# Performance work log

Hardware: AMD Instinct MI355X
Metric: run time of the kernel (lower is better)

Reference implementation:

```python
import jax, jax.numpy as jnp
import numpy as np

B, S, D_IN, D_OUT, H = 2, 2048, 1024, 1024, 16
HEAD = D_OUT // H

def setup_inputs() -> dict:
    key = jax.random.key(0)
    ks = jax.random.split(key, 5)
    scale = 0.02
    return {
        "x": jax.random.normal(ks[0], (B, S, D_IN), dtype=jnp.float32),
        "Wq": jax.random.normal(ks[1], (D_OUT, D_IN), dtype=jnp.float32) * scale,
        "Wk": jax.random.normal(ks[2], (D_OUT, D_IN), dtype=jnp.float32) * scale,
        "Wv": jax.random.normal(ks[3], (D_OUT, D_IN), dtype=jnp.float32) * scale,
        "Wo": jax.random.normal(ks[4], (D_OUT, D_OUT), dtype=jnp.float32) * scale,
        "bo": jnp.zeros((D_OUT,), dtype=jnp.float32),
    }

def reference(x, Wq, Wk, Wv, Wo, bo):
    b, n, _ = x.shape
    # linear projections (torch Linear: y = x @ W.T)
    q = (x @ Wq.T).reshape(b, n, H, HEAD).transpose(0, 2, 1, 3)  # [b,h,n,d]
    k = (x @ Wk.T).reshape(b, n, H, HEAD).transpose(0, 2, 1, 3)
    v = (x @ Wv.T).reshape(b, n, H, HEAD).transpose(0, 2, 1, 3)
    scores = jnp.einsum('bhqd,bhkd->bhqk', q, k)  # [b,h,n,n]
    causal = jnp.triu(jnp.ones((n, n), dtype=bool), k=1)
    scores = jnp.where(causal, -jnp.inf, scores)
    # NOTE: original scales by sqrt(d_out**0.5) == d_out**0.25 (faithful quirk)
    inv_scale = jnp.float32(1.0 / (D_OUT ** 0.25))
    attn = jax.nn.softmax(scores * inv_scale, axis=-1)
    ctx = jnp.einsum('bhqk,bhkd->bhqd', attn, v)  # [b,h,n,d]
    ctx = ctx.transpose(0, 2, 1, 3).reshape(b, n, D_OUT)
    return ctx @ Wo.T + bo
```

## Files before the change

### kernel.cpp

```cpp
#include <hip/hip_runtime.h>

#define NB 2
#define NH 16
#define SEQ 2048
#define DM 1024
#define HD 64
#define MT (NB * SEQ)

typedef __attribute__((ext_vector_type(8))) short bf16x8;
typedef __attribute__((ext_vector_type(4))) float f32x4;
typedef __attribute__((ext_vector_type(8))) unsigned short ushort8;

__device__ __forceinline__ unsigned short f2bf(float f) {
  union { float f; unsigned u; } v; v.f = f;
  return (unsigned short)((v.u + 0x7fffu + ((v.u >> 16) & 1u)) >> 16);
}

__device__ __forceinline__ void gld_lds16(const unsigned short* g, unsigned short* l) {
  __builtin_amdgcn_global_load_lds((const __attribute__((address_space(1))) unsigned int*)g,
                                   (__attribute__((address_space(3))) unsigned int*)l, 16, 0, 0);
}

__global__ __launch_bounds__(256) void cvt_all(const float* __restrict__ x,
                                               const float* __restrict__ wq,
                                               const float* __restrict__ wk,
                                               const float* __restrict__ wv,
                                               const float* __restrict__ wo,
                                               unsigned short* __restrict__ dst) {
  const int XO = (MT * DM) / 8;
  const int WO = (DM * DM) / 8;
  int i = blockIdx.x * 256 + threadIdx.x;
  const float* src; int base;
  if (i < XO)               { src = x;  base = 0; }
  else if (i < XO + WO)     { src = wq; base = XO; }
  else if (i < XO + 2 * WO) { src = wk; base = XO + WO; }
  else if (i < XO + 3 * WO) { src = wv; base = XO + 2 * WO; }
  else                      { src = wo; base = XO + 3 * WO; }
  const float4* s4 = (const float4*)(src) + (size_t)(i - base) * 2;
  float4 f0 = s4[0], f1 = s4[1];
  ushort8 u;
  u[0] = f2bf(f0.x); u[1] = f2bf(f0.y); u[2] = f2bf(f0.z); u[3] = f2bf(f0.w);
  u[4] = f2bf(f1.x); u[5] = f2bf(f1.y); u[6] = f2bf(f1.z); u[7] = f2bf(f1.w);
  *((ushort8*)dst + i) = u;
}

#define QSCALE 0.2550565444f

__global__ __launch_bounds__(128, 2) void gemm_qkv(const unsigned short* __restrict__ xb,
                                                   const unsigned short* __restrict__ wcat,
                                                   unsigned short* __restrict__ qb,
                                                   unsigned short* __restrict__ kb,
                                                   unsigned short* __restrict__ vtb) {
  __shared__ unsigned short As[128 * 64], Bs[128 * 64];
  int m0 = blockIdx.y * 128, n0 = blockIdx.x * 128;
  int tid = threadIdx.x, lane = tid & 63, l15 = lane & 15, quad = lane >> 4, w = tid >> 6;
  const unsigned short* A = xb + (size_t)m0 * DM;
  const unsigned short* B = wcat + (size_t)n0 * DM;

  int gofs[8];
#pragma unroll
  for (int it = 0; it < 8; ++it) {
    int c = tid + it * 128;
    int r = c >> 3, pos = c & 7;
    gofs[it] = r * DM + ((pos ^ (r & 7)) * 8);
  }

  f32x4 acc[8][4];
#pragma unroll
  for (int j = 0; j < 8; ++j)
#pragma unroll
    for (int i = 0; i < 4; ++i) acc[j][i] = (f32x4){0.f, 0.f, 0.f, 0.f};

  for (int k0 = 0; k0 < DM; k0 += 64) {
#pragma unroll
    for (int it = 0; it < 8; ++it)
      gld_lds16(A + k0 + gofs[it], As + (tid + it * 128) * 8);
#pragma unroll
    for (int it = 0; it < 8; ++it)
      gld_lds16(B + k0 + gofs[it], Bs + (tid + it * 128) * 8);
    __syncthreads();
#pragma unroll
    for (int s = 0; s < 2; ++s) {
      bf16x8 fa[4];
#pragma unroll
      for (int i = 0; i < 4; ++i) {
        int row = w * 64 + i * 16 + l15, sw = row & 7;
        fa[i] = *(const bf16x8*)(As + row * 64 + (((quad + 4 * s) ^ sw) * 8));
      }
#pragma unroll
      for (int j = 0; j < 8; ++j) {
        int row = j * 16 + l15, sw = row & 7;
        bf16x8 fb = *(const bf16x8*)(Bs + row * 64 + (((quad + 4 * s) ^ sw) * 8));
#pragma unroll
        for (int i = 0; i < 4; ++i)
          acc[j][i] = __builtin_amdgcn_mfma_f32_16x16x32_bf16(fb, fa[i], acc[j][i], 0, 0, 0);
      }
    }
    __syncthreads();
  }

  int mat = n0 >> 10;
#pragma unroll
  for (int j = 0; j < 8; ++j) {
#pragma unroll
    for (int i = 0; i < 4; ++i) {
      int n = n0 + j * 16 + quad * 4;
      int m = m0 + w * 64 + i * 16 + l15;
      int bi = m >> 11, s = m & 2047;
      int c = n & 1023, h = c >> 6, d0 = c & 63;
      if (mat == 2) {
#pragma unroll
        for (int reg = 0; reg < 4; ++reg)
          vtb[((size_t)((bi * NH + h) * HD + d0 + reg)) * SEQ + s] = f2bf(acc[j][i][reg]);
      } else {
        unsigned short* dst = (mat == 0) ? qb : kb;
        float sc = (mat == 0) ? QSCALE : 1.0f;
        ushort4 u;
        u.x = f2bf(acc[j][i][0] * sc); u.y = f2bf(acc[j][i][1] * sc);
        u.z = f2bf(acc[j][i][2] * sc); u.w = f2bf(acc[j][i][3] * sc);
        *(ushort4*)(dst + ((size_t)((bi * NH + h) * SEQ + s)) * HD + d0) = u;
      }
    }
  }
}

#define LP 136
#define LDK 72
#define LV 136

__global__ __launch_bounds__(512, 4) void attn_kernel(const unsigned short* __restrict__ qb,
                                                      const unsigned short* __restrict__ kb,
                                                      const unsigned short* __restrict__ vtb,
                                                      unsigned short* __restrict__ ctx) {
  __shared__ unsigned short Ps[128 * LP];
  __shared__ unsigned short Ks[128 * LDK];
  __shared__ unsigned short Vts[64 * LV];
  int bx = blockIdx.x, h = blockIdx.y, bi = blockIdx.z;
  int qst = bi ? (15 - bx) : bx;
  int q0 = qst * 128;
  int tid = threadIdx.x, lane = tid & 63, l15 = lane & 15, quad = lane >> 4, w = tid >> 6;

  const unsigned short* qbase = qb + ((size_t)(bi * NH + h) * SEQ + q0) * HD;
  const unsigned short* kbase = kb + ((size_t)(bi * NH + h) * SEQ) * HD;
  const unsigned short* vbase = vtb + ((size_t)(bi * NH + h) * HD) * SEQ;

  {
    int c = tid, r = c >> 3, cc = (c & 7) * 8;
    *(int4*)(Ps + r * LP + cc) = *(const int4*)(qbase + (size_t)r * HD + cc);
    c = tid + 512; r = c >> 3; cc = (c & 7) * 8;
    *(int4*)(Ps + r * LP + cc) = *(const int4*)(qbase + (size_t)r * HD + cc);
  }
  int kr = tid >> 3, kc = (tid & 7) * 8;
  int vr = tid >> 4, vc = (tid & 15) * 8;
  const unsigned short* kS0 = kbase + (size_t)kr * HD + kc;
  const unsigned short* kS1 = kS0 + (size_t)64 * HD;
  const unsigned short* vS0 = vbase + (size_t)vr * SEQ + vc;
  const unsigned short* vS1 = vS0 + (size_t)32 * SEQ;
  int4 kreg0 = *(const int4*)kS0, kreg1 = *(const int4*)kS1;
  int4 vreg0 = *(const int4*)vS0, vreg1 = *(const int4*)vS1;
  unsigned short* Kd0 = Ks + kr * LDK + kc;
  unsigned short* Kd1 = Kd0 + 64 * LDK;
  unsigned short* Vd0 = Vts + vr * LV + vc;
  unsigned short* Vd1 = Vd0 + 32 * LV;
  __syncthreads();

  bf16x8 aq0 = *(const bf16x8*)(Ps + (w * 16 + l15) * LP + 8 * quad);
  bf16x8 aq1 = *(const bf16x8*)(Ps + (w * 16 + l15) * LP + 32 + 8 * quad);

  union { uint4 q; bf16x8 v; } onesu;
  onesu.q = make_uint4(0x3F803F80u, 0x3F803F80u, 0x3F803F80u, 0x3F803F80u);
  const bf16x8 ones = onesu.v;

  f32x4 Oacc[4];
#pragma unroll
  for (int i = 0; i < 4; ++i) Oacc[i] = (f32x4){0.f, 0.f, 0.f, 0.f};
  f32x4 lacc = (f32x4){0.f, 0.f, 0.f, 0.f};
  int q0w = q0 + w * 16;
  int nt = qst + 1;
  unsigned short* Prow = Ps + (w * 16 + quad * 4) * LP + l15;

  for (int j = 0; j < nt; ++j) {
    __syncthreads();
    *(int4*)Kd0 = kreg0; *(int4*)Kd1 = kreg1;
    *(int4*)Vd0 = vreg0; *(int4*)Vd1 = vreg1;
    __syncthreads();
    if (j + 1 < nt) {
      size_t ko = (size_t)(j + 1) * 128 * HD;
      int vo = (j + 1) * 128;
      kreg0 = *(const int4*)(kS0 + ko); kreg1 = *(const int4*)(kS1 + ko);
      vreg0 = *(const int4*)(vS0 + vo); vreg1 = *(const int4*)(vS1 + vo);
    }
    bool diag = (j == nt - 1);
    int ns_hi = diag ? w : 7;
    int s_hi = ns_hi >> 1;

    if (!diag) {
#pragma unroll
      for (int ns = 0; ns < 8; ++ns) {
        bf16x8 bk0 = *(const bf16x8*)(Ks + (ns * 16 + l15) * LDK + 8 * quad);
        bf16x8 bk1 = *(const bf16x8*)(Ks + (ns * 16 + l15) * LDK + 32 + 8 * quad);
        f32x4 s = (f32x4){0.f, 0.f, 0.f, 0.f};
        s = __builtin_amdgcn_mfma_f32_16x16x32_bf16(aq0, bk0, s, 0, 0, 0);
        s = __builtin_amdgcn_mfma_f32_16x16x32_bf16(aq1, bk1, s, 0, 0, 0);
#pragma unroll
        for (int reg = 0; reg < 4; ++reg) {
          float p = __builtin_amdgcn_exp2f(s[reg]);
          union { float f; unsigned u; } pu; pu.f = p;
          Prow[reg * LP + ns * 16] = (unsigned short)(pu.u >> 16);
        }
      }
    } else {
      int kv0 = j * 128;
#pragma unroll
      for (int ns = 0; ns < 8; ++ns) {
        if (ns > ns_hi) break;
        bf16x8 bk0 = *(const bf16x8*)(Ks + (ns * 16 + l15) * LDK + 8 * quad);
        bf16x8 bk1 = *(const bf16x8*)(Ks + (ns * 16 + l15) * LDK + 32 + 8 * quad);
        f32x4 s = (f32x4){0.f, 0.f, 0.f, 0.f};
        s = __builtin_amdgcn_mfma_f32_16x16x32_bf16(aq0, bk0, s, 0, 0, 0);
        s = __builtin_amdgcn_mfma_f32_16x16x32_bf16(aq1, bk1, s, 0, 0, 0);
        bool m = (ns == ns_hi);
#pragma unroll
        for (int reg = 0; reg < 4; ++reg) {
          float xv = s[reg];
          if (m) {
            int kvg = kv0 + ns * 16 + l15;
            int qg = q0w + quad * 4 + reg;
            if (kvg > qg) xv = -INFINITY;
          }
          float p = __builtin_amdgcn_exp2f(xv);
          union { float f; unsigned u; } pu; pu.f = p;
          Prow[reg * LP + ns * 16] = (unsigned short)(pu.u >> 16);
        }
      }
      if (!(ns_hi & 1)) {
#pragma unroll
        for (int reg = 0; reg < 4; ++reg)
          Prow[reg * LP + (ns_hi + 1) * 16] = 0;
      }
    }

#pragma unroll
    for (int step = 0; step < 4; ++step) {
      if (step > s_hi) break;
      bf16x8 pa = *(const bf16x8*)(Ps + (w * 16 + l15) * LP + 8 * quad + 32 * step);
      lacc = __builtin_amdgcn_mfma_f32_16x16x32_bf16(ones, pa, lacc, 0, 0, 0);
#pragma unroll
      for (int nd = 0; nd < 4; ++nd) {
        bf16x8 bv = *(const bf16x8*)(Vts + (nd * 16 + l15) * LV + 8 * quad + 32 * step);
        Oacc[nd] = __builtin_amdgcn_mfma_f32_16x16x32_bf16(bv, pa, Oacc[nd], 0, 0, 0);
      }
    }
  }

  float rl = 1.0f / lacc[0];
  int s = q0w + l15;
#pragma unroll
  for (int nd = 0; nd < 4; ++nd) {
    ushort4 u;
    u.x = f2bf(Oacc[nd][0] * rl); u.y = f2bf(Oacc[nd][1] * rl);
    u.z = f2bf(Oacc[nd][2] * rl); u.w = f2bf(Oacc[nd][3] * rl);
    *(ushort4*)(ctx + ((size_t)(bi * SEQ + s)) * DM + h * HD + nd * 16 + quad * 4) = u;
  }
}

__global__ __launch_bounds__(256, 2) void gemm_out(const unsigned short* __restrict__ ctx,
                                                   const unsigned short* __restrict__ wob,
                                                   const float* __restrict__ bo,
                                                   float* __restrict__ out) {
  __shared__ unsigned short As[64 * 64], Bs[128 * 64];
  int m0 = blockIdx.y * 64, n0 = blockIdx.x * 128;
  int tid = threadIdx.x, lane = tid & 63, l15 = lane & 15, quad = lane >> 4, w = tid >> 6;
  int wm = (w >> 1) * 32, wn = (w & 1) * 64;
  const unsigned short* A = ctx + (size_t)m0 * DM;
  const unsigned short* B = wob + (size_t)n0 * DM;

  int goA[2], goB[4];
#pragma unroll
  for (int it = 0; it < 2; ++it) {
    int c = tid + it * 256, r = c >> 3, pos = c & 7;
    goA[it] = r * DM + ((pos ^ (r & 7)) * 8);
  }
#pragma unroll
  for (int it = 0; it < 4; ++it) {
    int c = tid + it * 256, r = c >> 3, pos = c & 7;
    goB[it] = r * DM + ((pos ^ (r & 7)) * 8);
  }

  f32x4 acc[4][2];
#pragma unroll
  for (int j = 0; j < 4; ++j)
#pragma unroll
    for (int i = 0; i < 2; ++i) acc[j][i] = (f32x4){0.f, 0.f, 0.f, 0.f};

  for (int k0 = 0; k0 < DM; k0 += 64) {
#pragma unroll
    for (int it = 0; it < 2; ++it)
      gld_lds16(A + k0 + goA[it], As + (tid + it * 256) * 8);
#pragma unroll
    for (int it = 0; it < 4; ++it)
      gld_lds16(B + k0 + goB[it], Bs + (tid + it * 256) * 8);
    __syncthreads();
#pragma unroll
    for (int s = 0; s < 2; ++s) {
      bf16x8 fa[2];
#pragma unroll
      for (int i = 0; i < 2; ++i) {
        int row = wm + i * 16 + l15, sw = row & 7;
        fa[i] = *(const bf16x8*)(As + row * 64 + (((quad + 4 * s) ^ sw) * 8));
      }
#pragma unroll
      for (int j = 0; j < 4; ++j) {
        int row = wn + j * 16 + l15, sw = row & 7;
        bf16x8 fb = *(const bf16x8*)(Bs + row * 64 + (((quad + 4 * s) ^ sw) * 8));
#pragma unroll
        for (int i = 0; i < 2; ++i)
          acc[j][i] = __builtin_amdgcn_mfma_f32_16x16x32_bf16(fb, fa[i], acc[j][i], 0, 0, 0);
      }
    }
    __syncthreads();
  }

#pragma unroll
  for (int j = 0; j < 4; ++j)
#pragma unroll
    for (int i = 0; i < 2; ++i) {
      int n = n0 + wn + j * 16 + quad * 4;
      int m = m0 + wm + i * 16 + l15;
      float4 bv = *(const float4*)(bo + n);
      float4 o;
      o.x = acc[j][i][0] + bv.x; o.y = acc[j][i][1] + bv.y;
      o.z = acc[j][i][2] + bv.z; o.w = acc[j][i][3] + bv.w;
      *(float4*)(out + (size_t)m * DM + n) = o;
    }
}

extern "C" void kernel_launch(void* const* d_in, const int* in_sizes, int n_in,
                              void* d_out, int out_size, void* d_ws, size_t ws_size,
                              hipStream_t stream) {
  const float* x  = (const float*)d_in[0];
  const float* Wq = (const float*)d_in[1];
  const float* Wk = (const float*)d_in[2];
  const float* Wv = (const float*)d_in[3];
  const float* Wo = (const float*)d_in[4];
  const float* bo = (const float*)d_in[5];
  float* out = (float*)d_out;

  unsigned short* ws = (unsigned short*)d_ws;
  unsigned short* xb   = ws;
  unsigned short* ctx  = ws;
  unsigned short* wcat = ws + (size_t)MT * DM;
  unsigned short* wob  = wcat + (size_t)3 * DM * DM;
  unsigned short* qb   = wob + (size_t)DM * DM;
  unsigned short* kb   = qb + (size_t)MT * DM;
  unsigned short* vtb  = kb + (size_t)MT * DM;

  int total8 = (MT * DM + 4 * DM * DM) / 8;
  cvt_all<<<total8 / 256, 256, 0, stream>>>(x, Wq, Wk, Wv, Wo, ws);

  gemm_qkv<<<dim3(24, 32), 128, 0, stream>>>(xb, wcat, qb, kb, vtb);
  attn_kernel<<<dim3(16, NH, NB), 512, 0, stream>>>(qb, kb, vtb, ctx);
  gemm_out<<<dim3(8, 64), 256, 0, stream>>>(ctx, wob, bo, out);
}
```

Baseline: 168.8 us.

## Load GEMM B-operand fragments directly from global into registers, bypassing LDS

In both the QKV projection GEMM and the output GEMM, the weight (B) operand is no longer staged through shared memory. Each thread now loads its MFMA fragments straight from global memory into registers, while the activation (A) tile still goes through LDS. The output GEMM is also retiled to 128 threads with 128x64 tiles and a different grid shape. This cuts LDS traffic and shared memory per block, which may raise occupancy, but it adds uncoalesced-ish global loads and more register pressure. Every block and every wave in a block now re-reads the same weight rows from global memory or cache.

```diff
diff --git a/kernel.cpp b/kernel.cpp
--- a/kernel.cpp
+++ b/kernel.cpp
@@ -51,11 +51,10 @@
                                                    unsigned short* __restrict__ qb,
                                                    unsigned short* __restrict__ kb,
                                                    unsigned short* __restrict__ vtb) {
-  __shared__ unsigned short As[128 * 64], Bs[128 * 64];
+  __shared__ unsigned short As[128 * 64];
   int m0 = blockIdx.y * 128, n0 = blockIdx.x * 128;
   int tid = threadIdx.x, lane = tid & 63, l15 = lane & 15, quad = lane >> 4, w = tid >> 6;
   const unsigned short* A = xb + (size_t)m0 * DM;
-  const unsigned short* B = wcat + (size_t)n0 * DM;
 
   int gofs[8];
 #pragma unroll
@@ -64,6 +63,10 @@
     int r = c >> 3, pos = c & 7;
     gofs[it] = r * DM + ((pos ^ (r & 7)) * 8);
   }
+  const unsigned short* bptr[8];
+#pragma unroll
+  for (int j = 0; j < 8; ++j)
+    bptr[j] = wcat + (size_t)(n0 + j * 16 + l15) * DM + quad * 8;
 
   f32x4 acc[8][4];
 #pragma unroll
@@ -75,9 +78,12 @@
 #pragma unroll
     for (int it = 0; it < 8; ++it)
       gld_lds16(A + k0 + gofs[it], As + (tid + it * 128) * 8);
-#pragma unroll
-    for (int it = 0; it < 8; ++it)
-      gld_lds16(B + k0 + gofs[it], Bs + (tid + it * 128) * 8);
+    bf16x8 fb[8][2];
+#pragma unroll
+    for (int j = 0; j < 8; ++j)
+#pragma unroll
+      for (int s = 0; s < 2; ++s)
+        fb[j][s] = *(const bf16x8*)(bptr[j] + k0 + s * 32);
     __syncthreads();
 #pragma unroll
     for (int s = 0; s < 2; ++s) {
@@ -88,13 +94,10 @@
         fa[i] = *(const bf16x8*)(As + row * 64 + (((quad + 4 * s) ^ sw) * 8));
       }
 #pragma unroll
-      for (int j = 0; j < 8; ++j) {
-        int row = j * 16 + l15, sw = row & 7;
-        bf16x8 fb = *(const bf16x8*)(Bs + row * 64 + (((quad + 4 * s) ^ sw) * 8));
+      for (int j = 0; j < 8; ++j)
 #pragma unroll
         for (int i = 0; i < 4; ++i)
-          acc[j][i] = __builtin_amdgcn_mfma_f32_16x16x32_bf16(fb, fa[i], acc[j][i], 0, 0, 0);
-      }
+          acc[j][i] = __builtin_amdgcn_mfma_f32_16x16x32_bf16(fb[j][s], fa[i], acc[j][i], 0, 0, 0);
     }
     __syncthreads();
   }
@@ -264,59 +267,57 @@
   }
 }
 
-__global__ __launch_bounds__(256, 2) void gemm_out(const unsigned short* __restrict__ ctx,
+__global__ __launch_bounds__(128, 2) void gemm_out(const unsigned short* __restrict__ ctx,
                                                    const unsigned short* __restrict__ wob,
                                                    const float* __restrict__ bo,
                                                    float* __restrict__ out) {
-  __shared__ unsigned short As[64 * 64], Bs[128 * 64];
-  int m0 = blockIdx.y * 64, n0 = blockIdx.x * 128;
+  __shared__ unsigned short As[128 * 64];
+  int n0 = blockIdx.x * 64, m0 = blockIdx.y * 128;
   int tid = threadIdx.x, lane = tid & 63, l15 = lane & 15, quad = lane >> 4, w = tid >> 6;
-  int wm = (w >> 1) * 32, wn = (w & 1) * 64;
   const unsigned short* A = ctx + (size_t)m0 * DM;
-  const unsigned short* B = wob + (size_t)n0 * DM;
-
-  int goA[2], goB[4];
-#pragma unroll
-  for (int it = 0; it < 2; ++it) {
-    int c = tid + it * 256, r = c >> 3, pos = c & 7;
-    goA[it] = r * DM + ((pos ^ (r & 7)) * 8);
-  }
-#pragma unroll
-  for (int it = 0; it < 4; ++it) {
-    int c = tid + it * 256, r = c >> 3, pos = c & 7;
-    goB[it] = r * DM + ((pos ^ (r & 7)) * 8);
-  }
-
-  f32x4 acc[4][2];
+
+  int gofs[8];
+#pragma unroll
+  for (int it = 0; it < 8; ++it) {
+    int c = tid + it * 128;
+    int r = c >> 3, pos = c & 7;
+    gofs[it] = r * DM + ((pos ^ (r & 7)) * 8);
+  }
+  const unsigned short* bptr[4];
 #pragma unroll
   for (int j = 0; j < 4; ++j)
-#pragma unroll
-    for (int i = 0; i < 2; ++i) acc[j][i] = (f32x4){0.f, 0.f, 0.f, 0.f};
+    bptr[j] = wob + (size_t)(n0 + j * 16 + l15) * DM + quad * 8;
+
+  f32x4 acc[4][4];
+#pragma unroll
+  for (int j = 0; j < 4; ++j)
+#pragma unroll
+    for (int i = 0; i < 4; ++i) acc[j][i] = (f32x4){0.f, 0.f, 0.f, 0.f};
 
   for (int k0 = 0; k0 < DM; k0 += 64) {
 #pragma unroll
-    for (int it = 0; it < 2; ++it)
-      gld_lds16(A + k0 + goA[it], As + (tid + it * 256) * 8);
-#pragma unroll
-    for (int it = 0; it < 4; ++it)
-      gld_lds16(B + k0 + goB[it], Bs + (tid + it * 256) * 8);
+    for (int it = 0; it < 8; ++it)
+      gld_lds16(A + k0 + gofs[it], As + (tid + it * 128) * 8);
+    bf16x8 fb[4][2];
+#pragma unroll
+    for (int j = 0; j < 4; ++j)
+#pragma unroll
+      for (int s = 0; s < 2; ++s)
+        fb[j][s] = *(const bf16x8*)(bptr[j] + k0 + s * 32);
     __syncthreads();
 #pragma unroll
     for (int s = 0; s < 2; ++s) {
-      bf16x8 fa[2];
-#pragma unroll
-      for (int i = 0; i < 2; ++i) {
-        int row = wm + i * 16 + l15, sw = row & 7;
+      bf16x8 fa[4];
+#pragma unroll
+      for (int i = 0; i < 4; ++i) {
+        int row = w * 64 + i * 16 + l15, sw = row & 7;
         fa[i] = *(const bf16x8*)(As + row * 64 + (((quad + 4 * s) ^ sw) * 8));
       }
 #pragma unroll
-      for (int j = 0; j < 4; ++j) {
-        int row = wn + j * 16 + l15, sw = row & 7;
-        bf16x8 fb = *(const bf16x8*)(Bs + row * 64 + (((quad + 4 * s) ^ sw) * 8));
-#pragma unroll
-        for (int i = 0; i < 2; ++i)
-          acc[j][i] = __builtin_amdgcn_mfma_f32_16x16x32_bf16(fb, fa[i], acc[j][i], 0, 0, 0);
-      }
+      for (int j = 0; j < 4; ++j)
+#pragma unroll
+        for (int i = 0; i < 4; ++i)
+          acc[j][i] = __builtin_amdgcn_mfma_f32_16x16x32_bf16(fb[j][s], fa[i], acc[j][i], 0, 0, 0);
     }
     __syncthreads();
   }
@@ -324,9 +325,9 @@
 #pragma unroll
   for (int j = 0; j < 4; ++j)
 #pragma unroll
-    for (int i = 0; i < 2; ++i) {
-      int n = n0 + wn + j * 16 + quad * 4;
-      int m = m0 + wm + i * 16 + l15;
+    for (int i = 0; i < 4; ++i) {
+      int n = n0 + j * 16 + quad * 4;
+      int m = m0 + w * 64 + i * 16 + l15;
       float4 bv = *(const float4*)(bo + n);
       float4 o;
       o.x = acc[j][i][0] + bv.x; o.y = acc[j][i][1] + bv.y;
@@ -360,5 +361,5 @@
 
   gemm_qkv<<<dim3(24, 32), 128, 0, stream>>>(xb, wcat, qb, kb, vtb);
   attn_kernel<<<dim3(16, NH, NB), 512, 0, stream>>>(qb, kb, vtb, ctx);
-  gemm_out<<<dim3(8, 64), 256, 0, stream>>>(ctx, wob, bo, out);
-}
+  gemm_out<<<dim3(16, 32), 128, 0, stream>>>(ctx, wob, bo, out);
+}
```

Result: slower. 200.3 us (+18.7%).
